# Performance work log

Hardware: AMD Instinct MI355X
Metric: run time of the kernel (lower is better)

## Reference

```python
import jax, jax.numpy as jnp
import numpy as np

B, C, H, W, J = 4, 32, 128, 240, 15
ORIG_W, ORIG_H = 1920, 1080


def _make_K(key, b, orig_w, orig_h):
    k1, k2, k3, k4 = jax.random.split(key, 4)
    fx = 1100.0 + 50.0 * jax.random.normal(k1, (b,))
    fy = 1100.0 + 50.0 * jax.random.normal(k2, (b,))
    cx = orig_w / 2.0 + 20.0 * jax.random.normal(k3, (b,))
    cy = orig_h / 2.0 + 20.0 * jax.random.normal(k4, (b,))
    K = jnp.zeros((b, 3, 3), dtype=jnp.float32)
    K = K.at[:, 0, 0].set(fx).at[:, 1, 1].set(fy)
    K = K.at[:, 0, 2].set(cx).at[:, 1, 2].set(cy).at[:, 2, 2].set(1.0)
    return K


def _make_rt(key, b):
    # well-conditioned homogeneous transform: rotation (QR) + translation
    k1, k2 = jax.random.split(key)
    R, _ = jnp.linalg.qr(jax.random.normal(k1, (b, 3, 3)))
    t = 0.5 * jax.random.normal(k2, (b, 3))
    M = jnp.tile(jnp.eye(4, dtype=jnp.float32)[None], (b, 1, 1))
    M = M.at[:, :3, :3].set(R.astype(jnp.float32)).at[:, :3, 3].set(t)
    return M


def setup_inputs() -> dict:
    key = jax.random.key(0)
    ks = jax.random.split(key, 7)
    pred_depth = jax.random.uniform(ks[0], (B, 1, H, W), minval=1.0, maxval=6.0, dtype=jnp.float32)
    filter_mask = jax.random.randint(ks[1], (J, B, H, W), 0, 2).astype(jnp.int32)
    K_matrix = _make_K(ks[2], B, ORIG_W, ORIG_H)
    M_matrix = _make_rt(ks[3], B)
    diff = (0.05 * jax.random.normal(ks[4], (B, 12))).astype(jnp.float32)
    trans_matrix = _make_rt(ks[5], B)
    feature_input = jax.random.normal(ks[6], (B, C, H, W), dtype=jnp.float32)
    return dict(pred_depth=pred_depth, filter_mask=filter_mask, K_matrix=K_matrix,
                M_matrix=M_matrix, diff=diff, trans_matrix=trans_matrix,
                feature_input=feature_input, orig_W=ORIG_W, orig_H=ORIG_H)


def reference(pred_depth, filter_mask, K_matrix, M_matrix, diff, trans_matrix, feature_input, orig_W, orig_H):
    b, _, h, w = pred_depth.shape
    c = feature_input.shape[1]
    hw = h * w
    depth = pred_depth.reshape(b, hw)  # squeeze(1) + flatten

    # pixel grid: x_cor[h,w] = (w+71)*(orig_W/480), y_cor[h,w] = h*(orig_H/H)
    x = (jnp.arange(w, dtype=jnp.float32) + 71.0) * (orig_W / 480.0)
    y = jnp.arange(h, dtype=jnp.float32) * (orig_H / h)
    xg = jnp.broadcast_to(x[None, :], (h, w)).reshape(-1)
    yg = jnp.broadcast_to(y[:, None], (h, w)).reshape(-1)
    cor_2d = jnp.stack([xg, yg, jnp.ones_like(xg)], axis=0)  # [3, HW]

    Kinv = jnp.linalg.inv(K_matrix)
    norm_2d = jnp.einsum('bij,jp->bpi', Kinv, cor_2d)  # [B, HW, 3]
    x_bak = norm_2d[..., 0]  # [B, HW]
    y_bak = norm_2d[..., 1]

    d = lambda i: diff[:, i][:, None]  # [B,1] broadcast against [B,HW]
    xd, yd = x_bak, y_bak
    for _ in range(5):  # fixed-count iterative undistortion
        r2 = xd * xd + yd * yd
        icdist = (1.0 + ((d(7) * r2 + d(6)) * r2 + d(5)) * r2) / \
                 (1.0 + ((d(4) * r2 + d(1)) * r2 + d(0)) * r2)
        deltaX = 2.0 * d(2) * xd * yd + d(3) * (r2 + 2.0 * xd * xd) + d(8) * r2 + d(9) * r2 * r2
        deltaY = d(2) * (r2 + 2.0 * yd * yd) + 2.0 * d(3) * xd * yd + d(10) * r2 + d(11) * r2 * r2
        xd = (x_bak - deltaX) * icdist
        yd = (y_bak - deltaY) * icdist

    xd = xd * depth
    yd = yd * depth
    depth_cam = jnp.stack([xd, yd, depth, jnp.ones_like(depth)], axis=-1)  # [B, HW, 4]

    # point_panoptic = (trans @ inv(M)) @ depth_cam^T, keep xyz
    T = jnp.einsum('bij,bjk->bik', trans_matrix, jnp.linalg.inv(M_matrix))
    point_panoptic = jnp.einsum('bij,bpj->bpi', T, depth_cam)[..., :3]  # [B, HW, 3]

    feat = feature_input.reshape(b, c, hw).transpose(0, 2, 1)  # [B, HW, C]
    pc = jnp.concatenate([point_panoptic, feat], axis=-1)  # [B, HW, 3+C]

    # dense masked equivalent of per-joint/per-batch ragged gather:
    # out[j,b,p] = pc[b,p] if mask[j,b,p]==1 else 0
    mask = filter_mask.reshape(filter_mask.shape[0], b, hw)
    out = pc[None] * mask[..., None].astype(pc.dtype)  # [J, B, HW, 3+C]
    return out
```

## Files before the change

kernel.cpp:

```cpp
#include <hip/hip_runtime.h>

#define HW_  (128*240)
#define W_   240
#define H_   128
#define B_   4
#define C_   32
#define J_   15
#define TILE 128
#define NT_  256
#define NSLOT (TILE*35/4)
#define JSTRIDE ((size_t)B_*HW_*35)
#define WS_PER_B 21

typedef float vfloat4 __attribute__((ext_vector_type(4)));

__global__ void setup_kernel(const float* __restrict__ K,
                             const float* __restrict__ M,
                             const float* __restrict__ trans,
                             float* __restrict__ ws) {
    int b = threadIdx.x;
    if (b >= B_) return;

    float a[3][6];
    for (int i = 0; i < 3; i++) {
        for (int j = 0; j < 3; j++) {
            a[i][j]     = K[b * 9 + i * 3 + j];
            a[i][3 + j] = (i == j) ? 1.0f : 0.0f;
        }
    }
    for (int col = 0; col < 3; col++) {
        int piv = col; float mx = fabsf(a[col][col]);
        for (int r = col + 1; r < 3; r++) {
            float v = fabsf(a[r][col]);
            if (v > mx) { mx = v; piv = r; }
        }
        if (piv != col) {
            for (int j = 0; j < 6; j++) { float t = a[col][j]; a[col][j] = a[piv][j]; a[piv][j] = t; }
        }
        float inv = 1.0f / a[col][col];
        for (int j = 0; j < 6; j++) a[col][j] *= inv;
        for (int r = 0; r < 3; r++) {
            if (r == col) continue;
            float f = a[r][col];
            for (int j = 0; j < 6; j++) a[r][j] -= f * a[col][j];
        }
    }
    for (int i = 0; i < 3; i++)
        for (int j = 0; j < 3; j++)
            ws[b * WS_PER_B + i * 3 + j] = a[i][3 + j];

    float m[4][8];
    for (int i = 0; i < 4; i++) {
        for (int j = 0; j < 4; j++) {
            m[i][j]     = M[b * 16 + i * 4 + j];
            m[i][4 + j] = (i == j) ? 1.0f : 0.0f;
        }
    }
    for (int col = 0; col < 4; col++) {
        int piv = col; float mx = fabsf(m[col][col]);
        for (int r = col + 1; r < 4; r++) {
            float v = fabsf(m[r][col]);
            if (v > mx) { mx = v; piv = r; }
        }
        if (piv != col) {
            for (int j = 0; j < 8; j++) { float t = m[col][j]; m[col][j] = m[piv][j]; m[piv][j] = t; }
        }
        float inv = 1.0f / m[col][col];
        for (int j = 0; j < 8; j++) m[col][j] *= inv;
        for (int r = 0; r < 4; r++) {
            if (r == col) continue;
            float f = m[r][col];
            for (int j = 0; j < 8; j++) m[r][j] -= f * m[col][j];
        }
    }
    for (int i = 0; i < 3; i++) {
        for (int k = 0; k < 4; k++) {
            float s = trans[b * 16 + i * 4 + 0] * m[0][4 + k];
            s += trans[b * 16 + i * 4 + 1] * m[1][4 + k];
            s += trans[b * 16 + i * 4 + 2] * m[2][4 + k];
            s += trans[b * 16 + i * 4 + 3] * m[3][4 + k];
            ws[b * WS_PER_B + 9 + i * 4 + k] = s;
        }
    }
}

__global__ __launch_bounds__(NT_) void points_kernel(
    const float* __restrict__ dep,
    const int*   __restrict__ mask,
    const float* __restrict__ feat,
    const float* __restrict__ diff,
    const float* __restrict__ ws,
    const int*   __restrict__ origW,
    const int*   __restrict__ origH,
    float*       __restrict__ out)
{
    __shared__ __align__(16) float pc_s[TILE * 35];
    __shared__ int bits_s[TILE + 1];

    const int b   = blockIdx.y;
    const int p0  = blockIdx.x * TILE;
    const int tid = threadIdx.x;

    const float* fbase = feat + (size_t)b * C_ * HW_ + p0;
    for (int idx = tid; idx < C_ * TILE; idx += NT_) {
        int c  = idx >> 7;
        int pl = idx & (TILE - 1);
        pc_s[pl * 35 + 3 + c] = fbase[(size_t)c * HW_ + pl];
    }
    if (tid < TILE) {
        const int* mbase = mask + (size_t)b * HW_ + p0 + tid;
        int bits = 0;
        #pragma unroll
        for (int j = 0; j < J_; j++)
            bits |= (mbase[(size_t)j * B_ * HW_] & 1) << j;
        bits_s[tid] = bits;

        const float* w = ws + b * WS_PER_B;
        const float k00 = w[0], k01 = w[1], k02 = w[2];
        const float k10 = w[3], k11 = w[4], k12 = w[5];
        const float sW = (float)origW[0] / 480.0f;
        const float sH = (float)origH[0] / (float)H_;

        int p  = p0 + tid;
        int hh = p / W_;
        int wi = p - hh * W_;
        float x = ((float)wi + 71.0f) * sW;
        float y = (float)hh * sH;

        float x_bak = k00 * x + k01 * y + k02;
        float y_bak = k10 * x + k11 * y + k12;

        const float* d = diff + b * 12;
        float d0 = d[0], d1 = d[1], d2 = d[2], d3 = d[3], d4 = d[4], d5 = d[5];
        float d6 = d[6], d7 = d[7], d8 = d[8], d9 = d[9], d10 = d[10], d11 = d[11];

        float xd = x_bak, yd = y_bak;
        #pragma unroll
        for (int it = 0; it < 5; it++) {
            float r2  = xd * xd + yd * yd;
            float num = 1.0f + ((d7 * r2 + d6) * r2 + d5) * r2;
            float den = 1.0f + ((d4 * r2 + d1) * r2 + d0) * r2;
            float icd = num / den;
            float dX = 2.0f * d2 * xd * yd + d3 * (r2 + 2.0f * xd * xd) + d8 * r2 + d9 * r2 * r2;
            float dY = d2 * (r2 + 2.0f * yd * yd) + 2.0f * d3 * xd * yd + d10 * r2 + d11 * r2 * r2;
            xd = (x_bak - dX) * icd;
            yd = (y_bak - dY) * icd;
        }
        float depth = dep[(size_t)b * HW_ + p];
        xd *= depth;
        yd *= depth;
        const float* T = w + 9;
        pc_s[tid * 35 + 0] = T[0] * xd + T[1] * yd + T[2]  * depth + T[3];
        pc_s[tid * 35 + 1] = T[4] * xd + T[5] * yd + T[6]  * depth + T[7];
        pc_s[tid * 35 + 2] = T[8] * xd + T[9] * yd + T[10] * depth + T[11];
    }
    __syncthreads();

    float* base0 = out + (size_t)b * HW_ * 35 + (size_t)p0 * 35;
    for (int i4 = tid; i4 < NSLOT; i4 += NT_) {
        int e   = i4 << 2;
        int pA  = e / 35;
        int rem = e - pA * 35;
        int r   = 35 - rem;
        vfloat4 v = *((const vfloat4*)&pc_s[e]);
        int bitsA = bits_s[pA];
        int bitsB = bits_s[pA + 1];
        int b0 = bitsA;
        int b1 = (r > 1) ? bitsA : bitsB;
        int b2 = (r > 2) ? bitsA : bitsB;
        int b3 = (r > 3) ? bitsA : bitsB;
        float* dst = base0 + e;
        #pragma unroll
        for (int j = 0; j < J_; j++) {
            vfloat4 o;
            o.x = ((b0 >> j) & 1) ? v.x : 0.0f;
            o.y = ((b1 >> j) & 1) ? v.y : 0.0f;
            o.z = ((b2 >> j) & 1) ? v.z : 0.0f;
            o.w = ((b3 >> j) & 1) ? v.w : 0.0f;
            *((vfloat4*)(dst + (size_t)j * JSTRIDE)) = o;
        }
    }
}

extern "C" void kernel_launch(void* const* d_in, const int* in_sizes, int n_in,
                              void* d_out, int out_size, void* d_ws, size_t ws_size,
                              hipStream_t stream) {
    const float* dep   = (const float*)d_in[0];
    const int*   maskp = (const int*)  d_in[1];
    const float* K     = (const float*)d_in[2];
    const float* M     = (const float*)d_in[3];
    const float* diff  = (const float*)d_in[4];
    const float* trans = (const float*)d_in[5];
    const float* feat  = (const float*)d_in[6];
    const int*   oW    = (const int*)  d_in[7];
    const int*   oH    = (const int*)  d_in[8];
    float* out = (float*)d_out;
    float* ws  = (float*)d_ws;

    setup_kernel<<<1, 64, 0, stream>>>(K, M, trans, ws);

    dim3 grid(HW_ / TILE, B_);
    points_kernel<<<grid, NT_, 0, stream>>>(dep, maskp, feat, diff, ws, oW, oH, out);
}
```

Measured before the change: 299.1 us.

## Fold matrix-inverse setup into points kernel and vectorize feature loads

Removes the separate single-block setup kernel. Each block's thread 0 now computes K^-1 and trans·M^-1 into shared memory, and an extra barrier publishes them before the projection math. The feature tile load now uses float4 global reads, scattered into the 35-wide shared rows. This drops one launch and its serialization in exchange for redundant per-block setup work, which adds latency to thread 0 before the barrier.

After: 293.4 us. Within noise of the previous version (-1.9%).

```diff
diff --git a/kernel.cpp b/kernel.cpp
--- a/kernel.cpp
+++ b/kernel.cpp
@@ -10,102 +10,98 @@
 #define NT_  256
 #define NSLOT (TILE*35/4)
 #define JSTRIDE ((size_t)B_*HW_*35)
-#define WS_PER_B 21
 
 typedef float vfloat4 __attribute__((ext_vector_type(4)));
-
-__global__ void setup_kernel(const float* __restrict__ K,
-                             const float* __restrict__ M,
-                             const float* __restrict__ trans,
-                             float* __restrict__ ws) {
-    int b = threadIdx.x;
-    if (b >= B_) return;
-
-    float a[3][6];
-    for (int i = 0; i < 3; i++) {
-        for (int j = 0; j < 3; j++) {
-            a[i][j]     = K[b * 9 + i * 3 + j];
-            a[i][3 + j] = (i == j) ? 1.0f : 0.0f;
-        }
-    }
-    for (int col = 0; col < 3; col++) {
-        int piv = col; float mx = fabsf(a[col][col]);
-        for (int r = col + 1; r < 3; r++) {
-            float v = fabsf(a[r][col]);
-            if (v > mx) { mx = v; piv = r; }
-        }
-        if (piv != col) {
-            for (int j = 0; j < 6; j++) { float t = a[col][j]; a[col][j] = a[piv][j]; a[piv][j] = t; }
-        }
-        float inv = 1.0f / a[col][col];
-        for (int j = 0; j < 6; j++) a[col][j] *= inv;
-        for (int r = 0; r < 3; r++) {
-            if (r == col) continue;
-            float f = a[r][col];
-            for (int j = 0; j < 6; j++) a[r][j] -= f * a[col][j];
-        }
-    }
-    for (int i = 0; i < 3; i++)
-        for (int j = 0; j < 3; j++)
-            ws[b * WS_PER_B + i * 3 + j] = a[i][3 + j];
-
-    float m[4][8];
-    for (int i = 0; i < 4; i++) {
-        for (int j = 0; j < 4; j++) {
-            m[i][j]     = M[b * 16 + i * 4 + j];
-            m[i][4 + j] = (i == j) ? 1.0f : 0.0f;
-        }
-    }
-    for (int col = 0; col < 4; col++) {
-        int piv = col; float mx = fabsf(m[col][col]);
-        for (int r = col + 1; r < 4; r++) {
-            float v = fabsf(m[r][col]);
-            if (v > mx) { mx = v; piv = r; }
-        }
-        if (piv != col) {
-            for (int j = 0; j < 8; j++) { float t = m[col][j]; m[col][j] = m[piv][j]; m[piv][j] = t; }
-        }
-        float inv = 1.0f / m[col][col];
-        for (int j = 0; j < 8; j++) m[col][j] *= inv;
-        for (int r = 0; r < 4; r++) {
-            if (r == col) continue;
-            float f = m[r][col];
-            for (int j = 0; j < 8; j++) m[r][j] -= f * m[col][j];
-        }
-    }
-    for (int i = 0; i < 3; i++) {
-        for (int k = 0; k < 4; k++) {
-            float s = trans[b * 16 + i * 4 + 0] * m[0][4 + k];
-            s += trans[b * 16 + i * 4 + 1] * m[1][4 + k];
-            s += trans[b * 16 + i * 4 + 2] * m[2][4 + k];
-            s += trans[b * 16 + i * 4 + 3] * m[3][4 + k];
-            ws[b * WS_PER_B + 9 + i * 4 + k] = s;
-        }
-    }
-}
 
 __global__ __launch_bounds__(NT_) void points_kernel(
     const float* __restrict__ dep,
     const int*   __restrict__ mask,
     const float* __restrict__ feat,
     const float* __restrict__ diff,
-    const float* __restrict__ ws,
+    const float* __restrict__ K,
+    const float* __restrict__ M,
+    const float* __restrict__ trans,
     const int*   __restrict__ origW,
     const int*   __restrict__ origH,
     float*       __restrict__ out)
 {
     __shared__ __align__(16) float pc_s[TILE * 35];
     __shared__ int bits_s[TILE + 1];
+    __shared__ float mats_s[21];
 
     const int b   = blockIdx.y;
     const int p0  = blockIdx.x * TILE;
     const int tid = threadIdx.x;
 
+    if (tid == 0) {
+        float a[3][6];
+        for (int i = 0; i < 3; i++)
+            for (int j = 0; j < 3; j++) {
+                a[i][j]     = K[b * 9 + i * 3 + j];
+                a[i][3 + j] = (i == j) ? 1.0f : 0.0f;
+            }
+        for (int col = 0; col < 3; col++) {
+            int piv = col; float mx = fabsf(a[col][col]);
+            for (int r = col + 1; r < 3; r++) {
+                float v = fabsf(a[r][col]);
+                if (v > mx) { mx = v; piv = r; }
+            }
+            if (piv != col)
+                for (int j = 0; j < 6; j++) { float t = a[col][j]; a[col][j] = a[piv][j]; a[piv][j] = t; }
+            float inv = 1.0f / a[col][col];
+            for (int j = 0; j < 6; j++) a[col][j] *= inv;
+            for (int r = 0; r < 3; r++) {
+                if (r == col) continue;
+                float f = a[r][col];
+                for (int j = 0; j < 6; j++) a[r][j] -= f * a[col][j];
+            }
+        }
+        for (int i = 0; i < 3; i++)
+            for (int j = 0; j < 3; j++)
+                mats_s[i * 3 + j] = a[i][3 + j];
+
+        float m[4][8];
+        for (int i = 0; i < 4; i++)
+            for (int j = 0; j < 4; j++) {
+                m[i][j]     = M[b * 16 + i * 4 + j];
+                m[i][4 + j] = (i == j) ? 1.0f : 0.0f;
+            }
+        for (int col = 0; col < 4; col++) {
+            int piv = col; float mx = fabsf(m[col][col]);
+            for (int r = col + 1; r < 4; r++) {
+                float v = fabsf(m[r][col]);
+                if (v > mx) { mx = v; piv = r; }
+            }
+            if (piv != col)
+                for (int j = 0; j < 8; j++) { float t = m[col][j]; m[col][j] = m[piv][j]; m[piv][j] = t; }
+            float inv = 1.0f / m[col][col];
+            for (int j = 0; j < 8; j++) m[col][j] *= inv;
+            for (int r = 0; r < 4; r++) {
+                if (r == col) continue;
+                float f = m[r][col];
+                for (int j = 0; j < 8; j++) m[r][j] -= f * m[col][j];
+            }
+        }
+        for (int i = 0; i < 3; i++)
+            for (int k = 0; k < 4; k++) {
+                float s = trans[b * 16 + i * 4 + 0] * m[0][4 + k]
+                        + trans[b * 16 + i * 4 + 1] * m[1][4 + k]
+                        + trans[b * 16 + i * 4 + 2] * m[2][4 + k]
+                        + trans[b * 16 + i * 4 + 3] * m[3][4 + k];
+                mats_s[9 + i * 4 + k] = s;
+            }
+    }
+
     const float* fbase = feat + (size_t)b * C_ * HW_ + p0;
-    for (int idx = tid; idx < C_ * TILE; idx += NT_) {
-        int c  = idx >> 7;
-        int pl = idx & (TILE - 1);
-        pc_s[pl * 35 + 3 + c] = fbase[(size_t)c * HW_ + pl];
+    for (int idx = tid; idx < C_ * TILE / 4; idx += NT_) {
+        int c = idx >> 5;
+        int q = idx & 31;
+        vfloat4 v = *((const vfloat4*)(fbase + (size_t)c * HW_ + 4 * q));
+        float* dst = &pc_s[(4 * q) * 35 + 3 + c];
+        dst[0]   = v.x;
+        dst[35]  = v.y;
+        dst[70]  = v.z;
+        dst[105] = v.w;
     }
     if (tid < TILE) {
         const int* mbase = mask + (size_t)b * HW_ + p0 + tid;
@@ -114,10 +110,12 @@
         for (int j = 0; j < J_; j++)
             bits |= (mbase[(size_t)j * B_ * HW_] & 1) << j;
         bits_s[tid] = bits;
+    }
+    __syncthreads();
 
-        const float* w = ws + b * WS_PER_B;
-        const float k00 = w[0], k01 = w[1], k02 = w[2];
-        const float k10 = w[3], k11 = w[4], k12 = w[5];
+    if (tid < TILE) {
+        const float k00 = mats_s[0], k01 = mats_s[1], k02 = mats_s[2];
+        const float k10 = mats_s[3], k11 = mats_s[4], k12 = mats_s[5];
         const float sW = (float)origW[0] / 480.0f;
         const float sH = (float)origH[0] / (float)H_;
 
@@ -149,7 +147,7 @@
         float depth = dep[(size_t)b * HW_ + p];
         xd *= depth;
         yd *= depth;
-        const float* T = w + 9;
+        const float* T = mats_s + 9;
         pc_s[tid * 35 + 0] = T[0] * xd + T[1] * yd + T[2]  * depth + T[3];
         pc_s[tid * 35 + 1] = T[4] * xd + T[5] * yd + T[6]  * depth + T[7];
         pc_s[tid * 35 + 2] = T[8] * xd + T[9] * yd + T[10] * depth + T[11];
@@ -195,10 +193,7 @@
     const int*   oW    = (const int*)  d_in[7];
     const int*   oH    = (const int*)  d_in[8];
     float* out = (float*)d_out;
-    float* ws  = (float*)d_ws;
-
-    setup_kernel<<<1, 64, 0, stream>>>(K, M, trans, ws);
 
     dim3 grid(HW_ / TILE, B_);
-    points_kernel<<<grid, NT_, 0, stream>>>(dep, maskp, feat, diff, ws, oW, oH, out);
+    points_kernel<<<grid, NT_, 0, stream>>>(dep, maskp, feat, diff, K, M, trans, oW, oH, out);
 }
```
